# Optimization experiments

Hardware: AMD Instinct MI355X
Metric: run time of the kernel (lower is better)

Reference implementation:

```python
import jax, jax.numpy as jnp
import numpy as np

B, N, D = 2, 2048, 768
H = 12
HD = D // H
SCALE = HD ** -0.5
EPS = 1e-8


def exp0(v, c):
    # Poincare exponential map at origin: tanh(sqrt(c)||v||) * v / (sqrt(c)||v||)
    sc = jnp.sqrt(c)
    n = jnp.sqrt(jnp.sum(v * v, axis=-1, keepdims=True))
    n = jnp.maximum(n, EPS)
    return jnp.tanh(sc * n) * v / (sc * n)


def log0(x, c):
    # Poincare log map at origin: artanh(sqrt(c)||x||) * x / (sqrt(c)||x||)
    sc = jnp.sqrt(c)
    n = jnp.sqrt(jnp.sum(x * x, axis=-1, keepdims=True))
    n = jnp.maximum(n, EPS)
    t = jnp.clip(sc * n, 0.0, 1.0 - 1e-7)
    return jnp.arctanh(t) * x / (sc * n)


def setup_inputs() -> dict:
    key = jax.random.key(0)
    k1, k2, k3 = jax.random.split(key, 3)
    c0 = 0.1
    x = jax.random.normal(k1, (B, N, D), dtype=jnp.float32)
    # rescale so sqrt(c)*||x|| = 0.5 -> valid points strictly inside the ball
    xn = jnp.sqrt(jnp.sum(x * x, axis=-1, keepdims=True))
    x = x * (0.5 / (np.sqrt(c0) * jnp.maximum(xn, EPS)))
    w_qkv = jax.random.normal(k2, (3 * D, D), dtype=jnp.float32) * (D ** -0.5)
    w_proj = jax.random.normal(k3, (D, D), dtype=jnp.float32) * (D ** -0.5)
    b_proj = jnp.zeros((D,), dtype=jnp.float32)
    curvature = jnp.asarray(c0, dtype=jnp.float32)
    return {"x": x, "w_qkv": w_qkv, "w_proj": w_proj, "b_proj": b_proj,
            "curvature": curvature}


def reference(x, w_qkv, w_proj, b_proj, curvature):
    c = curvature
    v = log0(x, c)                                   # [B,N,D] tangent vectors
    qkv = jnp.einsum('bnd,ed->bne', v, w_qkv)        # [B,N,3D]
    qkv = qkv.reshape(B, N, 3, H, HD).transpose(2, 0, 3, 1, 4)  # [3,B,H,N,HD]
    q, k, v_proj = qkv[0], qkv[1], qkv[2]
    # Map q,k back onto the manifold for the hyperbolic distance score
    qm = exp0(q, c)                                  # [B,H,N,HD]
    km = exp0(k, c)
    q_nsq = jnp.sum(qm * qm, axis=-1)                # [B,H,N]
    k_nsq = jnp.sum(km * km, axis=-1)                # [B,H,N]
    dot = jnp.einsum('bhnd,bhmd->bhnm', qm, km)      # [B,H,N,N]
    # ||q-k||^2 = ||q||^2 + ||k||^2 - 2 q.k  (avoids [B,H,N,N,HD] intermediate)
    diff_sq = jnp.maximum(q_nsq[..., :, None] + k_nsq[..., None, :] - 2.0 * dot, 0.0)
    q_cl = jnp.minimum(q_nsq, 0.99)
    k_cl = jnp.minimum(k_nsq, 0.99)
    denom = (1.0 - q_cl)[..., :, None] * (1.0 - k_cl)[..., None, :] + 1e-8
    inner = jnp.maximum(1.0 + 2.0 * diff_sq / denom, 1.0 + 1e-7)
    distances = jnp.arccosh(inner)                   # [B,H,N,N]
    scores = -distances * SCALE
    attn = jax.nn.softmax(scores, axis=-1)
    out = jnp.einsum('bhnm,bhmd->bhnd', attn, v_proj)
    out = out.transpose(0, 2, 1, 3).reshape(B, N, D)
    v_out = jnp.einsum('bnd,ed->bne', out, w_proj) + b_proj
    return exp0(v_out, c)                            # [B,N,D] on manifold
```

## Files before the change

kernel.cpp:

```cpp
#include <hip/hip_runtime.h>
#include <cmath>

#define ROWS 4096
#define DIM 768
#define QKV_COLS 2304
#define NHEAD 12
#define HEAD_DIM 64
#define SEQ 2048
#define PADK 72

static constexpr float SCALE_F = 0.125f;
static constexpr float EPS_F   = 1e-8f;

typedef __bf16 bfrag __attribute__((ext_vector_type(8)));
typedef float  f32x4 __attribute__((ext_vector_type(4)));

__device__ __forceinline__ float wave_sum64(float v) {
#pragma unroll
  for (int off = 1; off < 64; off <<= 1) v += __shfl_xor(v, off, 64);
  return v;
}

__device__ __forceinline__ unsigned short f2bf(float f) {
  unsigned u = __float_as_uint(f);
  u += 0x7fffu + ((u >> 16) & 1u);
  return (unsigned short)(u >> 16);
}

__device__ __forceinline__ void gl_lds16(const void* g, void* l) {
  __builtin_amdgcn_global_load_lds((const __attribute__((address_space(1))) void*)g,
                                   (__attribute__((address_space(3))) void*)l, 16, 0, 0);
}

__global__ __launch_bounds__(256) void conv_bf16(const float* __restrict__ src,
                                                 unsigned short* __restrict__ dst, int n) {
  const int i = (blockIdx.x * 256 + threadIdx.x) * 4;
  if (i < n) {
    const float4 v = *(const float4*)(src + i);
    ushort4 o;
    o.x = f2bf(v.x); o.y = f2bf(v.y); o.z = f2bf(v.z); o.w = f2bf(v.w);
    *(ushort4*)(dst + i) = o;
  }
}

__global__ __launch_bounds__(256) void log0_kernel(const float* __restrict__ x,
                                                   const float* __restrict__ cptr,
                                                   unsigned short* __restrict__ vout) {
  const int lane = threadIdx.x & 63;
  const int row  = (blockIdx.x << 2) + (threadIdx.x >> 6);
  const float* xr = x + (size_t)row * DIM;
  unsigned short* vr = vout + (size_t)row * DIM;
  float vals[12];
  float ss = 0.f;
#pragma unroll
  for (int i = 0; i < 12; ++i) {
    float t = xr[lane + (i << 6)];
    vals[i] = t;
    ss += t * t;
  }
  ss = wave_sum64(ss);
  const float sc  = sqrtf(cptr[0]);
  const float n   = fmaxf(sqrtf(ss), EPS_F);
  const float scn = sc * n;
  const float t   = fminf(scn, 1.0f - 1e-7f);
  const float f   = atanhf(t) / scn;
#pragma unroll
  for (int i = 0; i < 12; ++i) vr[lane + (i << 6)] = f2bf(vals[i] * f);
}

__global__ __launch_bounds__(256) void exp0_out_kernel(const float* __restrict__ vin,
                                                       const float* __restrict__ cptr,
                                                       float* __restrict__ outp) {
  const int lane = threadIdx.x & 63;
  const int row  = (blockIdx.x << 2) + (threadIdx.x >> 6);
  const float* vr = vin + (size_t)row * DIM;
  float* orow = outp + (size_t)row * DIM;
  float vals[12];
  float ss = 0.f;
#pragma unroll
  for (int i = 0; i < 12; ++i) {
    float t = vr[lane + (i << 6)];
    vals[i] = t;
    ss += t * t;
  }
  ss = wave_sum64(ss);
  const float sc  = sqrtf(cptr[0]);
  const float n   = fmaxf(sqrtf(ss), EPS_F);
  const float scn = sc * n;
  const float f   = tanhf(scn) / scn;
#pragma unroll
  for (int i = 0; i < 12; ++i) orow[lane + (i << 6)] = vals[i] * f;
}

__global__ __launch_bounds__(256) void gemm_nt_mfma(const unsigned short* __restrict__ A,
                                                    const unsigned short* __restrict__ B,
                                                    float* __restrict__ C,
                                                    int M, int Ncols, int K,
                                                    const float* __restrict__ bias) {
  __shared__ unsigned short As[128 * 32];
  __shared__ unsigned short Bs[128 * 32];
  const int tid = threadIdx.x;
  const int w = tid >> 6, lane = tid & 63;
  const int lq = lane & 15, quad = lane >> 4;
  const int wr = w >> 1, wc = w & 1;
  const int row0 = blockIdx.y << 7;
  const int col0 = blockIdx.x << 7;

  const int srow  = lane >> 2;
  const int skoff = (lane & 3) << 3;

  f32x4 acc[4][4];
#pragma unroll
  for (int i = 0; i < 4; ++i)
#pragma unroll
    for (int j = 0; j < 4; ++j) acc[i][j] = (f32x4){0.f, 0.f, 0.f, 0.f};

  for (int k0 = 0; k0 < K; k0 += 32) {
    __syncthreads();
#pragma unroll
    for (int q = 0; q < 2; ++q) {
      const int r = ((w << 1) + q) << 4;
      gl_lds16(A + (size_t)(row0 + r + srow) * K + k0 + skoff, &As[((w << 1) + q) << 9]);
      gl_lds16(B + (size_t)(col0 + r + srow) * K + k0 + skoff, &Bs[((w << 1) + q) << 9]);
    }
    __syncthreads();

    bfrag af[4], bfg[4];
#pragma unroll
    for (int i = 0; i < 4; ++i)
      af[i] = *(const bfrag*)&As[((wr << 6) + (i << 4) + lq) * 32 + (quad << 3)];
#pragma unroll
    for (int j = 0; j < 4; ++j)
      bfg[j] = *(const bfrag*)&Bs[((wc << 6) + (j << 4) + lq) * 32 + (quad << 3)];
#pragma unroll
    for (int i = 0; i < 4; ++i)
#pragma unroll
      for (int j = 0; j < 4; ++j)
        acc[i][j] = __builtin_amdgcn_mfma_f32_16x16x32_bf16(af[i], bfg[j], acc[i][j], 0, 0, 0);
  }

#pragma unroll
  for (int i = 0; i < 4; ++i) {
    const int crow = row0 + (wr << 6) + (i << 4) + (quad << 2);
#pragma unroll
    for (int j = 0; j < 4; ++j) {
      const int col = col0 + (wc << 6) + (j << 4) + lq;
      const float bj = bias ? bias[col] : 0.0f;
      float* cp = C + (size_t)crow * Ncols + col;
#pragma unroll
      for (int r = 0; r < 4; ++r)
        cp[(size_t)r * Ncols] = acc[i][j][r] + bj;
    }
  }
}

__global__ __launch_bounds__(256) void exp0_qk_prep(const float* __restrict__ qkv,
                                                    const float* __restrict__ cptr,
                                                    unsigned short* __restrict__ qh,
                                                    unsigned short* __restrict__ kh,
                                                    float2* __restrict__ qn2,
                                                    float2* __restrict__ kn2) {
  const int lane = threadIdx.x & 63;
  const int vec  = (blockIdx.x << 2) + (threadIdx.x >> 6);
  const int which = vec & 1;
  const int rest  = vec >> 1;
  const int h   = rest % NHEAD;
  const int row = rest / NHEAD;
  const int b = row >> 11, n = row & 2047;
  const int bh = b * NHEAD + h;
  const float t = qkv[(size_t)row * QKV_COLS + which * DIM + h * HEAD_DIM + lane];
  const float ss = wave_sum64(t * t);
  const float sc  = sqrtf(cptr[0]);
  const float nn  = fmaxf(sqrtf(ss), EPS_F);
  const float scn = sc * nn;
  const float f   = tanhf(scn) / scn;
  const float m   = t * f;
  unsigned short* dst = (which ? kh : qh) + ((size_t)bh * SEQ + n) * HEAD_DIM + lane;
  *dst = f2bf(m);
  if (lane == 0) {
    const float nrm = ss * f * f;
    const float rc  = 1.0f / (1.0f - fminf(nrm, 0.99f));
    (which ? kn2 : qn2)[(size_t)bh * SEQ + n] = make_float2(nrm, rc);
  }
}

__global__ __launch_bounds__(256) void v_transpose_prep(const float* __restrict__ qkv,
                                                        unsigned short* __restrict__ vth) {
  const int kt = blockIdx.x, h = blockIdx.y, b = blockIdx.z;
  const int bh = b * NHEAD + h;
  __shared__ unsigned short T[64 * PADK];
  const int tid = threadIdx.x;
  const int r  = tid >> 2;
  const int c0 = (tid & 3) << 4;
  const float* src = qkv + ((size_t)(b * SEQ + kt * 64 + r)) * QKV_COLS + 2 * DIM + h * HEAD_DIM + c0;
#pragma unroll
  for (int z = 0; z < 16; z += 4) {
    const float4 v = *(const float4*)(src + z);
    T[(c0 + z + 0) * PADK + r] = f2bf(v.x);
    T[(c0 + z + 1) * PADK + r] = f2bf(v.y);
    T[(c0 + z + 2) * PADK + r] = f2bf(v.z);
    T[(c0 + z + 3) * PADK + r] = f2bf(v.w);
  }
  __syncthreads();
  const int d  = tid >> 2;
  const int k0 = (tid & 3) << 4;
  unsigned short* dst = vth + ((size_t)bh * HEAD_DIM + d) * SEQ + (size_t)kt * 64 + k0;
  *(uint4*)dst       = *(const uint4*)&T[d * PADK + k0];
  *(uint4*)(dst + 8) = *(const uint4*)&T[d * PADK + k0 + 8];
}

__global__ __launch_bounds__(256) void flash_mfma(const unsigned short* __restrict__ qh,
                                                  const unsigned short* __restrict__ kh,
                                                  const unsigned short* __restrict__ vth,
                                                  const float2* __restrict__ qn2,
                                                  const float2* __restrict__ kn2,
                                                  unsigned short* __restrict__ attn_out) {
  const int qt = blockIdx.x, h = blockIdx.y, b = blockIdx.z;
  const int bh = b * NHEAD + h;
  const int tid = threadIdx.x;
  const int w = tid >> 6, lane = tid & 63;
  const int lq = lane & 15, quad = lane >> 4;

  __shared__ unsigned short Ks[64 * 64];
  __shared__ unsigned short Vt[64 * 64];
  __shared__ unsigned short Ps[64 * PADK];
  __shared__ float2 kn_s[64];

  const unsigned short* qbase = qh + ((size_t)bh * SEQ + (size_t)qt * 64) * HEAD_DIM;
  const float2* qnb = qn2 + (size_t)bh * SEQ + (size_t)qt * 64;
  const float2* knb = kn2 + (size_t)bh * SEQ;

  const int srow = tid >> 3, spos = tid & 7;
  const int sB = spos ^ (srow & 7);
  const char* kgsrc = (const char*)(kh + (size_t)bh * SEQ * HEAD_DIM) + (size_t)srow * 128 + sB * 16;
  const char* vgsrc = (const char*)(vth + (size_t)bh * HEAD_DIM * SEQ) + (size_t)srow * 4096 + sB * 16;

  bfrag aq[2];
#pragma unroll
  for (int khf = 0; khf < 2; ++khf)
    aq[khf] = *(const bfrag*)(qbase + (size_t)(w * 16 + lq) * HEAD_DIM + khf * 32 + quad * 8);

  float qn4[4], rq2[4];
#pragma unroll
  for (int i = 0; i < 4; ++i) {
    const float2 qq = qnb[w * 16 + quad * 4 + i];
    qn4[i] = qq.x;
    rq2[i] = 2.0f * qq.y;
  }

  f32x4 oacc[4];
#pragma unroll
  for (int d = 0; d < 4; ++d) oacc[d] = (f32x4){0.f, 0.f, 0.f, 0.f};
  float l4[4] = {0.f, 0.f, 0.f, 0.f};

  const int swz = (lq & 7);

  for (int kt = 0; kt < SEQ / 64; ++kt) {
    __syncthreads();
    gl_lds16(kgsrc,          (char*)Ks + w * 1024);
    gl_lds16(kgsrc + 4096,   (char*)Ks + 4096 + w * 1024);
    gl_lds16(vgsrc,          (char*)Vt + w * 1024);
    gl_lds16(vgsrc + 131072, (char*)Vt + 4096 + w * 1024);
    if (tid < 64) kn_s[tid] = knb[kt * 64 + tid];
    kgsrc += 8192;
    vgsrc += 128;
    __syncthreads();

    f32x4 s[4];
#pragma unroll
    for (int st = 0; st < 4; ++st) s[st] = (f32x4){0.f, 0.f, 0.f, 0.f};
#pragma unroll
    for (int khf = 0; khf < 2; ++khf)
#pragma unroll
      for (int st = 0; st < 4; ++st) {
        const bfrag bk = *(const bfrag*)&Ks[(st * 16 + lq) * 64 + (((khf << 2) + quad) ^ swz) * 8];
        s[st] = __builtin_amdgcn_mfma_f32_16x16x32_bf16(aq[khf], bk, s[st], 0, 0, 0);
      }

#pragma unroll
    for (int st = 0; st < 4; ++st) {
      const float2 kk = kn_s[st * 16 + lq];
#pragma unroll
      for (int i = 0; i < 4; ++i) {
        float t = fmaf(-2.0f, s[st][i], qn4[i] + kk.x);
        t = fmaxf(t, 0.0f);
        const float inner = fmaf(t, rq2[i] * kk.y, 1.0f);
        const float root = __builtin_amdgcn_sqrtf(fmaf(inner, inner, -1.0f));
        const float wgt = __builtin_amdgcn_exp2f(-0.125f * __builtin_amdgcn_logf(inner + root));
        const unsigned u = __float_as_uint(wgt);
        Ps[(w * 16 + quad * 4 + i) * PADK + st * 16 + lq] = (unsigned short)(u >> 16);
        l4[i] += __uint_as_float(u & 0xffff0000u);
      }
    }

#pragma unroll
    for (int khf = 0; khf < 2; ++khf) {
      const bfrag ap = *(const bfrag*)&Ps[(w * 16 + lq) * PADK + khf * 32 + quad * 8];
#pragma unroll
      for (int d = 0; d < 4; ++d) {
        const bfrag bv = *(const bfrag*)&Vt[(d * 16 + lq) * 64 + (((khf << 2) + quad) ^ swz) * 8];
        oacc[d] = __builtin_amdgcn_mfma_f32_16x16x32_bf16(ap, bv, oacc[d], 0, 0, 0);
      }
    }
  }

  float rl4[4];
#pragma unroll
  for (int i = 0; i < 4; ++i) {
    float s_ = l4[i];
    s_ += __shfl_xor(s_, 1, 64);
    s_ += __shfl_xor(s_, 2, 64);
    s_ += __shfl_xor(s_, 4, 64);
    s_ += __shfl_xor(s_, 8, 64);
    rl4[i] = __builtin_amdgcn_rcpf(s_);
  }
  unsigned short* ob = attn_out + ((size_t)b * SEQ + (size_t)qt * 64 + w * 16) * DIM + h * HEAD_DIM;
#pragma unroll
  for (int d = 0; d < 4; ++d)
#pragma unroll
    for (int i = 0; i < 4; ++i)
      ob[(size_t)(quad * 4 + i) * DIM + d * 16 + lq] = f2bf(oacc[d][i] * rl4[i]);
}

extern "C" void kernel_launch(void* const* d_in, const int* in_sizes, int n_in,
                              void* d_out, int out_size, void* d_ws, size_t ws_size,
                              hipStream_t stream) {
  const float* x      = (const float*)d_in[0];
  const float* w_qkv  = (const float*)d_in[1];
  const float* w_proj = (const float*)d_in[2];
  const float* b_proj = (const float*)d_in[3];
  const float* curv   = (const float*)d_in[4];
  float* outp = (float*)d_out;

  float* ws = (float*)d_ws;
  unsigned short* v_tan_bf = (unsigned short*)ws;
  unsigned short* attn_bf  = (unsigned short*)ws;
  float* qkv   = ws + 1572864;
  float* v_out = qkv;
  unsigned short* qh  = (unsigned short*)(qkv + 9437184);
  unsigned short* kh  = qh + 3145728;
  unsigned short* vth = kh + 3145728;
  unsigned short* wqkv_bf  = vth + 3145728;
  unsigned short* wproj_bf = wqkv_bf + 1769472;
  float2* qn2 = (float2*)(wproj_bf + 589824);
  float2* kn2 = qn2 + 49152;

  conv_bf16<<<dim3((1769472 / 4 + 255) / 256), dim3(256), 0, stream>>>(w_qkv, wqkv_bf, 1769472);
  conv_bf16<<<dim3((589824 / 4 + 255) / 256), dim3(256), 0, stream>>>(w_proj, wproj_bf, 589824);
  log0_kernel<<<dim3(ROWS / 4), dim3(256), 0, stream>>>(x, curv, v_tan_bf);
  gemm_nt_mfma<<<dim3(QKV_COLS / 128, ROWS / 128), dim3(256), 0, stream>>>(
      v_tan_bf, wqkv_bf, qkv, ROWS, QKV_COLS, DIM, nullptr);
  exp0_qk_prep<<<dim3(ROWS * NHEAD * 2 / 4), dim3(256), 0, stream>>>(qkv, curv, qh, kh,
                                                                     qn2, kn2);
  v_transpose_prep<<<dim3(SEQ / 64, NHEAD, 2), dim3(256), 0, stream>>>(qkv, vth);
  flash_mfma<<<dim3(SEQ / 64, NHEAD, 2), dim3(256), 0, stream>>>(qh, kh, vth, qn2,
                                                                 kn2, attn_bf);
  gemm_nt_mfma<<<dim3(DIM / 128, ROWS / 128), dim3(256), 0, stream>>>(
      attn_bf, wproj_bf, v_out, ROWS, DIM, DIM, b_proj);
  exp0_out_kernel<<<dim3(ROWS / 4), dim3(256), 0, stream>>>(v_out, curv, outp);
}
```

Before: 241.2 us.

## Merge prep kernels, load two key tiles per barrier, transpose score MFMA layout

Merges the two weight-conversion launches into one and fuses the q/k exp0 prep with the V transpose into a single kernel, cutting launch count. In the attention kernel, each sync round now stages 128 keys (two 64-key tiles), halving barriers. The score MFMA operands are swapped so each lane owns one query row, letting P be written as packed 8-byte stores and the row sum be reduced with fewer shuffles. It doubles LDS use per block, which may lower occupancy, and the fused prep kernel runs a serial 32-iteration loop per wave with one-element loads.

Measured after the change: 234.5 us. -2.8%, faster.

```diff
diff --git a/kernel.cpp b/kernel.cpp
--- a/kernel.cpp
+++ b/kernel.cpp
@@ -32,15 +32,20 @@
                                    (__attribute__((address_space(3))) void*)l, 16, 0, 0);
 }
 
-__global__ __launch_bounds__(256) void conv_bf16(const float* __restrict__ src,
-                                                 unsigned short* __restrict__ dst, int n) {
+__global__ __launch_bounds__(256) void conv_bf16_2(const float* __restrict__ a, int na,
+                                                   const float* __restrict__ b, int nb,
+                                                   unsigned short* __restrict__ da,
+                                                   unsigned short* __restrict__ db) {
   const int i = (blockIdx.x * 256 + threadIdx.x) * 4;
-  if (i < n) {
-    const float4 v = *(const float4*)(src + i);
-    ushort4 o;
-    o.x = f2bf(v.x); o.y = f2bf(v.y); o.z = f2bf(v.z); o.w = f2bf(v.w);
-    *(ushort4*)(dst + i) = o;
-  }
+  const float* s;
+  unsigned short* d;
+  int j;
+  if (i < na) { s = a; d = da; j = i; }
+  else { j = i - na; if (j >= nb) return; s = b; d = db; }
+  const float4 v = *(const float4*)(s + j);
+  ushort4 o;
+  o.x = f2bf(v.x); o.y = f2bf(v.y); o.z = f2bf(v.z); o.w = f2bf(v.w);
+  *(ushort4*)(d + j) = o;
 }
 
 __global__ __launch_bounds__(256) void log0_kernel(const float* __restrict__ x,
@@ -154,57 +159,53 @@
   }
 }
 
-__global__ __launch_bounds__(256) void exp0_qk_prep(const float* __restrict__ qkv,
-                                                    const float* __restrict__ cptr,
-                                                    unsigned short* __restrict__ qh,
-                                                    unsigned short* __restrict__ kh,
-                                                    float2* __restrict__ qn2,
-                                                    float2* __restrict__ kn2) {
-  const int lane = threadIdx.x & 63;
-  const int vec  = (blockIdx.x << 2) + (threadIdx.x >> 6);
-  const int which = vec & 1;
-  const int rest  = vec >> 1;
-  const int h   = rest % NHEAD;
-  const int row = rest / NHEAD;
-  const int b = row >> 11, n = row & 2047;
+__global__ __launch_bounds__(256) void qkv_prep(const float* __restrict__ qkv,
+                                                const float* __restrict__ cptr,
+                                                unsigned short* __restrict__ qh,
+                                                unsigned short* __restrict__ kh,
+                                                unsigned short* __restrict__ vth,
+                                                float2* __restrict__ qn2,
+                                                float2* __restrict__ kn2) {
+  const int qt = blockIdx.x, h = blockIdx.y, b = blockIdx.z;
   const int bh = b * NHEAD + h;
-  const float t = qkv[(size_t)row * QKV_COLS + which * DIM + h * HEAD_DIM + lane];
-  const float ss = wave_sum64(t * t);
-  const float sc  = sqrtf(cptr[0]);
-  const float nn  = fmaxf(sqrtf(ss), EPS_F);
-  const float scn = sc * nn;
-  const float f   = tanhf(scn) / scn;
-  const float m   = t * f;
-  unsigned short* dst = (which ? kh : qh) + ((size_t)bh * SEQ + n) * HEAD_DIM + lane;
-  *dst = f2bf(m);
-  if (lane == 0) {
-    const float nrm = ss * f * f;
-    const float rc  = 1.0f / (1.0f - fminf(nrm, 0.99f));
-    (which ? kn2 : qn2)[(size_t)bh * SEQ + n] = make_float2(nrm, rc);
-  }
-}
-
-__global__ __launch_bounds__(256) void v_transpose_prep(const float* __restrict__ qkv,
-                                                        unsigned short* __restrict__ vth) {
-  const int kt = blockIdx.x, h = blockIdx.y, b = blockIdx.z;
-  const int bh = b * NHEAD + h;
+  const int tid = threadIdx.x;
+  const int w = tid >> 6, lane = tid & 63;
+  const float sc = sqrtf(cptr[0]);
+
+  for (int t = 0; t < 32; ++t) {
+    const int vv = w * 32 + t;
+    const int which = vv & 1;
+    const int r = vv >> 1;
+    const int n = qt * 64 + r;
+    const float v = qkv[((size_t)(b * SEQ + n)) * QKV_COLS + which * DIM + h * HEAD_DIM + lane];
+    const float ss = wave_sum64(v * v);
+    const float nn = fmaxf(sqrtf(ss), EPS_F);
+    const float scn = sc * nn;
+    const float f = tanhf(scn) / scn;
+    (which ? kh : qh)[((size_t)bh * SEQ + n) * HEAD_DIM + lane] = f2bf(v * f);
+    if (lane == 0) {
+      const float nrm = ss * f * f;
+      (which ? kn2 : qn2)[(size_t)bh * SEQ + n] =
+          make_float2(nrm, 1.0f / (1.0f - fminf(nrm, 0.99f)));
+    }
+  }
+
   __shared__ unsigned short T[64 * PADK];
-  const int tid = threadIdx.x;
-  const int r  = tid >> 2;
+  const int r2 = tid >> 2;
   const int c0 = (tid & 3) << 4;
-  const float* src = qkv + ((size_t)(b * SEQ + kt * 64 + r)) * QKV_COLS + 2 * DIM + h * HEAD_DIM + c0;
+  const float* src = qkv + ((size_t)(b * SEQ + qt * 64 + r2)) * QKV_COLS + 2 * DIM + h * HEAD_DIM + c0;
 #pragma unroll
   for (int z = 0; z < 16; z += 4) {
     const float4 v = *(const float4*)(src + z);
-    T[(c0 + z + 0) * PADK + r] = f2bf(v.x);
-    T[(c0 + z + 1) * PADK + r] = f2bf(v.y);
-    T[(c0 + z + 2) * PADK + r] = f2bf(v.z);
-    T[(c0 + z + 3) * PADK + r] = f2bf(v.w);
+    T[(c0 + z + 0) * PADK + r2] = f2bf(v.x);
+    T[(c0 + z + 1) * PADK + r2] = f2bf(v.y);
+    T[(c0 + z + 2) * PADK + r2] = f2bf(v.z);
+    T[(c0 + z + 3) * PADK + r2] = f2bf(v.w);
   }
   __syncthreads();
   const int d  = tid >> 2;
   const int k0 = (tid & 3) << 4;
-  unsigned short* dst = vth + ((size_t)bh * HEAD_DIM + d) * SEQ + (size_t)kt * 64 + k0;
+  unsigned short* dst = vth + ((size_t)bh * HEAD_DIM + d) * SEQ + (size_t)qt * 64 + k0;
   *(uint4*)dst       = *(const uint4*)&T[d * PADK + k0];
   *(uint4*)(dst + 8) = *(const uint4*)&T[d * PADK + k0 + 8];
 }
@@ -221,10 +222,11 @@
   const int w = tid >> 6, lane = tid & 63;
   const int lq = lane & 15, quad = lane >> 4;
 
-  __shared__ unsigned short Ks[64 * 64];
-  __shared__ unsigned short Vt[64 * 64];
+  __shared__ unsigned short Ks[2 * 64 * 64];
+  __shared__ unsigned short Vt[2 * 64 * 64];
   __shared__ unsigned short Ps[64 * PADK];
-  __shared__ float2 kn_s[64];
+  __shared__ float knA[128], knB[128];
+  __shared__ float l_s[64];
 
   const unsigned short* qbase = qh + ((size_t)bh * SEQ + (size_t)qt * 64) * HEAD_DIM;
   const float2* qnb = qn2 + (size_t)bh * SEQ + (size_t)qt * 64;
@@ -240,80 +242,91 @@
   for (int khf = 0; khf < 2; ++khf)
     aq[khf] = *(const bfrag*)(qbase + (size_t)(w * 16 + lq) * HEAD_DIM + khf * 32 + quad * 8);
 
-  float qn4[4], rq2[4];
-#pragma unroll
-  for (int i = 0; i < 4; ++i) {
-    const float2 qq = qnb[w * 16 + quad * 4 + i];
-    qn4[i] = qq.x;
-    rq2[i] = 2.0f * qq.y;
-  }
+  const float2 qq = qnb[w * 16 + lq];
+  const float qnS = qq.x;
+  const float rqS = 2.0f * qq.y;
 
   f32x4 oacc[4];
 #pragma unroll
   for (int d = 0; d < 4; ++d) oacc[d] = (f32x4){0.f, 0.f, 0.f, 0.f};
-  float l4[4] = {0.f, 0.f, 0.f, 0.f};
-
-  const int swz = (lq & 7);
-
-  for (int kt = 0; kt < SEQ / 64; ++kt) {
+  float l = 0.0f;
+  const int swz = lq & 7;
+
+  for (int rd = 0; rd < SEQ / 128; ++rd) {
     __syncthreads();
-    gl_lds16(kgsrc,          (char*)Ks + w * 1024);
-    gl_lds16(kgsrc + 4096,   (char*)Ks + 4096 + w * 1024);
-    gl_lds16(vgsrc,          (char*)Vt + w * 1024);
-    gl_lds16(vgsrc + 131072, (char*)Vt + 4096 + w * 1024);
-    if (tid < 64) kn_s[tid] = knb[kt * 64 + tid];
-    kgsrc += 8192;
-    vgsrc += 128;
+    gl_lds16(kgsrc,                (char*)Ks + w * 1024);
+    gl_lds16(kgsrc + 4096,         (char*)Ks + 4096 + w * 1024);
+    gl_lds16(kgsrc + 8192,         (char*)Ks + 8192 + w * 1024);
+    gl_lds16(kgsrc + 12288,        (char*)Ks + 12288 + w * 1024);
+    gl_lds16(vgsrc,                (char*)Vt + w * 1024);
+    gl_lds16(vgsrc + 131072,       (char*)Vt + 4096 + w * 1024);
+    gl_lds16(vgsrc + 128,          (char*)Vt + 8192 + w * 1024);
+    gl_lds16(vgsrc + 131072 + 128, (char*)Vt + 12288 + w * 1024);
+    if (tid < 128) {
+      const float2 kv = knb[rd * 128 + tid];
+      knA[tid] = kv.x;
+      knB[tid] = kv.y;
+    }
+    kgsrc += 16384;
+    vgsrc += 256;
     __syncthreads();
 
-    f32x4 s[4];
-#pragma unroll
-    for (int st = 0; st < 4; ++st) s[st] = (f32x4){0.f, 0.f, 0.f, 0.f};
-#pragma unroll
-    for (int khf = 0; khf < 2; ++khf)
+#pragma unroll
+    for (int t = 0; t < 2; ++t) {
+      const unsigned short* KsT = &Ks[t * 4096];
+      const unsigned short* VtT = &Vt[t * 4096];
+
+      f32x4 s[4];
+#pragma unroll
+      for (int st = 0; st < 4; ++st) s[st] = (f32x4){0.f, 0.f, 0.f, 0.f};
+#pragma unroll
+      for (int khf = 0; khf < 2; ++khf)
+#pragma unroll
+        for (int st = 0; st < 4; ++st) {
+          const bfrag ak = *(const bfrag*)&KsT[(st * 16 + lq) * 64 + (((khf << 2) + quad) ^ swz) * 8];
+          s[st] = __builtin_amdgcn_mfma_f32_16x16x32_bf16(ak, aq[khf], s[st], 0, 0, 0);
+        }
+
 #pragma unroll
       for (int st = 0; st < 4; ++st) {
-        const bfrag bk = *(const bfrag*)&Ks[(st * 16 + lq) * 64 + (((khf << 2) + quad) ^ swz) * 8];
-        s[st] = __builtin_amdgcn_mfma_f32_16x16x32_bf16(aq[khf], bk, s[st], 0, 0, 0);
+        const f32x4 kna = *(const f32x4*)&knA[t * 64 + st * 16 + quad * 4];
+        const f32x4 knr = *(const f32x4*)&knB[t * 64 + st * 16 + quad * 4];
+        unsigned u[4];
+#pragma unroll
+        for (int i = 0; i < 4; ++i) {
+          float tt = fmaf(-2.0f, s[st][i], qnS + kna[i]);
+          tt = fmaxf(tt, 0.0f);
+          const float inner = fmaf(tt, rqS * knr[i], 1.0f);
+          const float root = __builtin_amdgcn_sqrtf(fmaf(inner, inner, -1.0f));
+          const float wgt = __builtin_amdgcn_exp2f(-0.125f * __builtin_amdgcn_logf(inner + root));
+          u[i] = __float_as_uint(wgt);
+          l += __uint_as_float(u[i] & 0xffff0000u);
+        }
+        uint2 pk;
+        pk.x = (u[0] >> 16) | (u[1] & 0xffff0000u);
+        pk.y = (u[2] >> 16) | (u[3] & 0xffff0000u);
+        *(uint2*)&Ps[(w * 16 + lq) * PADK + st * 16 + quad * 4] = pk;
       }
 
 #pragma unroll
-    for (int st = 0; st < 4; ++st) {
-      const float2 kk = kn_s[st * 16 + lq];
-#pragma unroll
-      for (int i = 0; i < 4; ++i) {
-        float t = fmaf(-2.0f, s[st][i], qn4[i] + kk.x);
-        t = fmaxf(t, 0.0f);
-        const float inner = fmaf(t, rq2[i] * kk.y, 1.0f);
-        const float root = __builtin_amdgcn_sqrtf(fmaf(inner, inner, -1.0f));
-        const float wgt = __builtin_amdgcn_exp2f(-0.125f * __builtin_amdgcn_logf(inner + root));
-        const unsigned u = __float_as_uint(wgt);
-        Ps[(w * 16 + quad * 4 + i) * PADK + st * 16 + lq] = (unsigned short)(u >> 16);
-        l4[i] += __uint_as_float(u & 0xffff0000u);
+      for (int khf = 0; khf < 2; ++khf) {
+        const bfrag ap = *(const bfrag*)&Ps[(w * 16 + lq) * PADK + khf * 32 + quad * 8];
+#pragma unroll
+        for (int d = 0; d < 4; ++d) {
+          const bfrag bv = *(const bfrag*)&VtT[(d * 16 + lq) * 64 + (((khf << 2) + quad) ^ swz) * 8];
+          oacc[d] = __builtin_amdgcn_mfma_f32_16x16x32_bf16(ap, bv, oacc[d], 0, 0, 0);
+        }
       }
     }
-
-#pragma unroll
-    for (int khf = 0; khf < 2; ++khf) {
-      const bfrag ap = *(const bfrag*)&Ps[(w * 16 + lq) * PADK + khf * 32 + quad * 8];
-#pragma unroll
-      for (int d = 0; d < 4; ++d) {
-        const bfrag bv = *(const bfrag*)&Vt[(d * 16 + lq) * 64 + (((khf << 2) + quad) ^ swz) * 8];
-        oacc[d] = __builtin_amdgcn_mfma_f32_16x16x32_bf16(ap, bv, oacc[d], 0, 0, 0);
-      }
-    }
-  }
-
+  }
+
+  l += __shfl_xor(l, 16, 64);
+  l += __shfl_xor(l, 32, 64);
+  if (quad == 0) l_s[w * 16 + lq] = l;
   float rl4[4];
 #pragma unroll
-  for (int i = 0; i < 4; ++i) {
-    float s_ = l4[i];
-    s_ += __shfl_xor(s_, 1, 64);
-    s_ += __shfl_xor(s_, 2, 64);
-    s_ += __shfl_xor(s_, 4, 64);
-    s_ += __shfl_xor(s_, 8, 64);
-    rl4[i] = __builtin_amdgcn_rcpf(s_);
-  }
+  for (int i = 0; i < 4; ++i) rl4[i] = __builtin_amdgcn_rcpf(l_s[w * 16 + quad * 4 + i]);
+
   unsigned short* ob = attn_out + ((size_t)b * SEQ + (size_t)qt * 64 + w * 16) * DIM + h * HEAD_DIM;
 #pragma unroll
   for (int d = 0; d < 4; ++d)
@@ -345,14 +358,13 @@
   float2* qn2 = (float2*)(wproj_bf + 589824);
   float2* kn2 = qn2 + 49152;
 
-  conv_bf16<<<dim3((1769472 / 4 + 255) / 256), dim3(256), 0, stream>>>(w_qkv, wqkv_bf, 1769472);
-  conv_bf16<<<dim3((589824 / 4 + 255) / 256), dim3(256), 0, stream>>>(w_proj, wproj_bf, 589824);
+  conv_bf16_2<<<dim3((2359296 / 4 + 255) / 256), dim3(256), 0, stream>>>(
+      w_qkv, 1769472, w_proj, 589824, wqkv_bf, wproj_bf);
   log0_kernel<<<dim3(ROWS / 4), dim3(256), 0, stream>>>(x, curv, v_tan_bf);
   gemm_nt_mfma<<<dim3(QKV_COLS / 128, ROWS / 128), dim3(256), 0, stream>>>(
       v_tan_bf, wqkv_bf, qkv, ROWS, QKV_COLS, DIM, nullptr);
-  exp0_qk_prep<<<dim3(ROWS * NHEAD * 2 / 4), dim3(256), 0, stream>>>(qkv, curv, qh, kh,
-                                                                     qn2, kn2);
-  v_transpose_prep<<<dim3(SEQ / 64, NHEAD, 2), dim3(256), 0, stream>>>(qkv, vth);
+  qkv_prep<<<dim3(SEQ / 64, NHEAD, 2), dim3(256), 0, stream>>>(qkv, curv, qh, kh, vth,
+                                                               qn2, kn2);
   flash_mfma<<<dim3(SEQ / 64, NHEAD, 2), dim3(256), 0, stream>>>(qh, kh, vth, qn2,
                                                                  kn2, attn_bf);
   gemm_nt_mfma<<<dim3(DIM / 128, ROWS / 128), dim3(256), 0, stream>>>(
```
